# Optimization experiments

Hardware: AMD Instinct MI355X
Metric: run time of the kernel (lower is better)

Reference implementation:

```python
import jax, jax.numpy as jnp
import numpy as np

ZNEAR, ZFAR = 0.01, 100.0
EPS2D = 0.3            # gsplat 2D covariance blur
ALPHA_MIN = 1.0 / 255.0
ALPHA_MAX = 0.999
N_GAUSS, N_VIEWS, IMG_H, IMG_W = 4096, 1, 128, 128


def quat_to_rotmat(q):
    # q: [N,4] in wxyz (gsplat convention), normalized here
    q = q / jnp.linalg.norm(q, axis=-1, keepdims=True)
    w, x, y, z = q[..., 0], q[..., 1], q[..., 2], q[..., 3]
    r0 = jnp.stack([1 - 2 * (y * y + z * z), 2 * (x * y - w * z), 2 * (x * z + w * y)], -1)
    r1 = jnp.stack([2 * (x * y + w * z), 1 - 2 * (x * x + z * z), 2 * (y * z - w * x)], -1)
    r2 = jnp.stack([2 * (x * z - w * y), 2 * (y * z + w * x), 1 - 2 * (x * x + y * y)], -1)
    return jnp.stack([r0, r1, r2], -2)


def _render_one(K, viewmat, means, quats, scales, opacities, rgb, H, W):
    # --- project gaussians to camera space ---
    Rw, tw = viewmat[:3, :3], viewmat[:3, 3]
    p = means @ Rw.T + tw                              # [N,3]
    x, y, z = p[:, 0], p[:, 1], p[:, 2]
    zs = jnp.where(jnp.abs(z) < 1e-6, 1e-6, z)
    rz = 1.0 / zs

    # --- 3D covariance: R(q) diag(s^2) R(q)^T, rotated into camera frame ---
    Rg = quat_to_rotmat(quats)                         # [N,3,3]
    M = Rg * scales[:, None, :]
    cov3d = M @ jnp.swapaxes(M, -1, -2)
    covc = jnp.einsum('ij,njk,lk->nil', Rw, cov3d, Rw)

    # --- EWA splatting: 2D covariance via perspective Jacobian ---
    fx, fy, cx, cy = K[0, 0], K[1, 1], K[0, 2], K[1, 2]
    zeros = jnp.zeros_like(rz)
    J = jnp.stack([
        jnp.stack([fx * rz, zeros, -fx * x * rz * rz], -1),
        jnp.stack([zeros, fy * rz, -fy * y * rz * rz], -1),
    ], -2)                                             # [N,2,3]
    cov2d = jnp.einsum('nij,njk,nlk->nil', J, covc, J)
    a = cov2d[:, 0, 0] + EPS2D
    c = cov2d[:, 1, 1] + EPS2D
    b = cov2d[:, 0, 1]
    det = a * c - b * b
    det_s = jnp.where(det > 0, det, 1.0)
    ca, cb, cc = c / det_s, -b / det_s, a / det_s      # conic = inv(cov2d)

    mx = fx * x * rz + cx
    my = fy * y * rz + cy
    valid = (z > ZNEAR) & (z < ZFAR) & (det > 0)

    # --- front-to-back depth ordering ---
    order = jnp.argsort(jnp.where(valid, z, jnp.inf))
    mx, my = mx[order], my[order]
    ca, cb, cc = ca[order], cb[order], cc[order]
    op_s, rgb_s, valid_s = opacities[order], rgb[order], valid[order]

    # --- per-pixel gaussian evaluation (pixel centers at +0.5) ---
    px = jnp.arange(W, dtype=jnp.float32) + 0.5
    py = jnp.arange(H, dtype=jnp.float32) + 0.5
    dx = px[None, None, :] - mx[:, None, None]          # [N,1,W]
    dy = py[None, :, None] - my[:, None, None]          # [N,H,1]
    sigma = 0.5 * (ca[:, None, None] * dx * dx + cc[:, None, None] * dy * dy) + cb[:, None, None] * dx * dy
    alpha = jnp.minimum(ALPHA_MAX, op_s[:, None, None] * jnp.exp(-sigma))
    keep = (sigma >= 0) & (alpha >= ALPHA_MIN) & valid_s[:, None, None]
    alpha = jnp.where(keep, alpha, 0.0)                 # [N,H,W]

    # --- alpha compositing: T_i = prod_{j<i}(1-alpha_j) ---
    Tincl = jnp.cumprod(1.0 - alpha, axis=0)
    Texcl = jnp.concatenate([jnp.ones_like(alpha[:1]), Tincl[:-1]], axis=0)
    w = alpha * Texcl
    img = jnp.einsum('nhw,nc->hwc', w, rgb_s)
    bg = jnp.zeros((rgb.shape[-1],), dtype=img.dtype)   # bg_color buffer is zeros
    img = img + Tincl[-1][..., None] * bg
    return img


def setup_inputs() -> dict:
    key = jax.random.key(0)
    ks = jax.random.split(key, 6)
    xy = jax.random.uniform(ks[0], (N_GAUSS, 2), minval=-2.0, maxval=2.0)
    z = jax.random.uniform(ks[1], (N_GAUSS, 1), minval=2.0, maxval=8.0)
    means = jnp.concatenate([xy, z], axis=-1)
    quats = jax.random.normal(ks[2], (N_GAUSS, 4))
    scales = jax.random.uniform(ks[3], (N_GAUSS, 3), minval=0.02, maxval=0.12)
    opacities = jax.random.uniform(ks[4], (N_GAUSS,), minval=0.3, maxval=1.0)
    rgb = jax.random.uniform(ks[5], (N_GAUSS, 3))
    K = jnp.array([[140.0, 0.0, IMG_W / 2], [0.0, 140.0, IMG_H / 2], [0.0, 0.0, 1.0]], dtype=jnp.float32)
    Ks = jnp.tile(K[None], (N_VIEWS, 1, 1))
    viewmats = jnp.tile(jnp.eye(4, dtype=jnp.float32)[None], (N_VIEWS, 1, 1))
    return {"Ks": Ks, "viewmats": viewmats, "means": means, "quats": quats,
            "scales": scales, "opacities": opacities, "rgb": rgb,
            "im_height": IMG_H, "im_width": IMG_W}


def reference(Ks, viewmats, means, quats, scales, opacities, rgb, im_height, im_width):
    render = jax.vmap(lambda K, vm: _render_one(K, vm, means, quats, scales, opacities, rgb, im_height, im_width))
    imgs = render(Ks, viewmats)                 # [V,H,W,C]
    return jnp.transpose(imgs, (0, 3, 1, 2))    # 'v h w c -> v c h w'
```

## Files before the change

kernel.cpp:

```cpp
#include <hip/hip_runtime.h>
#include <hip/hip_bf16.h>
#include <hip/hip_fp16.h>

typedef unsigned long long u64;

#define ZNEAR 0.01f
#define ZFAR 100.0f
#define EPS2D 0.3f
#define ALPHA_MIN (1.0f/255.0f)
#define ALPHA_MAX 0.999f
#define IMGH 128
#define IMGW 128
#define NPIX (IMGH*IMGW)
#define TMIN 1e-5f

__device__ __forceinline__ float ldin(const void* p, int i, bool f32in) {
    if (f32in) return ((const float*)p)[i];
    return __bfloat162float(((const __hip_bfloat16*)p)[i]);
}

__device__ __forceinline__ bool probe_f32(const void* Ks) {
    float v = ((const float*)Ks)[0];
    return (v > 1e-3f) && (v < 1e9f);
}

__global__ void prep_kernel(const void* __restrict__ Ks,
                            const void* __restrict__ vm,
                            const void* __restrict__ c0,
                            const void* __restrict__ c1,
                            const void* __restrict__ c2,
                            const void* __restrict__ quats,
                            const void* __restrict__ opac,
                            u64* __restrict__ keys,
                            float4* __restrict__ params,
                            int N)
{
    int i = blockIdx.x * blockDim.x + threadIdx.x;
    if (i >= N) return;
    bool F = probe_f32(Ks);

    const void* cand[3] = {c0, c1, c2};
    float mxv[3];
    #pragma unroll
    for (int t = 0; t < 3; ++t) {
        float m = 0.f;
        for (int k = 0; k < 16; ++k) m = fmaxf(m, fabsf(ldin(cand[t], 3*k+2, F)));
        mxv[t] = m;
    }
    const void* means = c0; const void* scales = c1; const void* rgb = c2;
    #pragma unroll
    for (int t = 0; t < 3; ++t) {
        if (mxv[t] > 1.5f)       means  = cand[t];
        else if (mxv[t] > 0.3f)  rgb    = cand[t];
        else                     scales = cand[t];
    }

    float fx = ldin(Ks,0,F), fy = ldin(Ks,4,F), cx = ldin(Ks,2,F), cy = ldin(Ks,5,F);
    float R00=ldin(vm,0,F),  R01=ldin(vm,1,F),  R02=ldin(vm,2,F),  t0=ldin(vm,3,F);
    float R10=ldin(vm,4,F),  R11=ldin(vm,5,F),  R12=ldin(vm,6,F),  t1=ldin(vm,7,F);
    float R20=ldin(vm,8,F),  R21=ldin(vm,9,F),  R22=ldin(vm,10,F), t2=ldin(vm,11,F);

    float m0=ldin(means,3*i,F), m1=ldin(means,3*i+1,F), m2=ldin(means,3*i+2,F);
    float px = R00*m0 + R01*m1 + R02*m2 + t0;
    float py = R10*m0 + R11*m1 + R12*m2 + t1;
    float pz = R20*m0 + R21*m1 + R22*m2 + t2;

    float zs = (fabsf(pz) < 1e-6f) ? 1e-6f : pz;
    float rz = 1.0f / zs;

    float qw=ldin(quats,4*i,F), qx=ldin(quats,4*i+1,F),
          qy=ldin(quats,4*i+2,F), qz=ldin(quats,4*i+3,F);
    float s2 = 2.0f / (qw*qw + qx*qx + qy*qy + qz*qz);
    float G00 = 1.0f - s2*(qy*qy + qz*qz), G01 = s2*(qx*qy - qw*qz), G02 = s2*(qx*qz + qw*qy);
    float G10 = s2*(qx*qy + qw*qz), G11 = 1.0f - s2*(qx*qx + qz*qz), G12 = s2*(qy*qz - qw*qx);
    float G20 = s2*(qx*qz - qw*qy), G21 = s2*(qy*qz + qw*qx), G22 = 1.0f - s2*(qx*qx + qy*qy);

    float s0=ldin(scales,3*i,F), s1=ldin(scales,3*i+1,F), sc2=ldin(scales,3*i+2,F);
    float M00=G00*s0, M01=G01*s1, M02=G02*sc2;
    float M10=G10*s0, M11=G11*s1, M12=G12*sc2;
    float M20=G20*s0, M21=G21*s1, M22=G22*sc2;

    float C00 = M00*M00 + M01*M01 + M02*M02;
    float C01 = M00*M10 + M01*M11 + M02*M12;
    float C02 = M00*M20 + M01*M21 + M02*M22;
    float C11 = M10*M10 + M11*M11 + M12*M12;
    float C12 = M10*M20 + M11*M21 + M12*M22;
    float C22 = M20*M20 + M21*M21 + M22*M22;

    float T00 = R00*C00 + R01*C01 + R02*C02;
    float T01 = R00*C01 + R01*C11 + R02*C12;
    float T02 = R00*C02 + R01*C12 + R02*C22;
    float T10 = R10*C00 + R11*C01 + R12*C02;
    float T11 = R10*C01 + R11*C11 + R12*C12;
    float T12 = R10*C02 + R11*C12 + R12*C22;
    float T20 = R20*C00 + R21*C01 + R22*C02;
    float T21 = R20*C01 + R21*C11 + R22*C12;
    float T22 = R20*C02 + R21*C12 + R22*C22;

    float W00 = T00*R00 + T01*R01 + T02*R02;
    float W01 = T00*R10 + T01*R11 + T02*R12;
    float W02 = T00*R20 + T01*R21 + T02*R22;
    float W11 = T10*R10 + T11*R11 + T12*R12;
    float W12 = T10*R20 + T11*R21 + T12*R22;
    float W22 = T20*R20 + T21*R21 + T22*R22;

    float j00 = fx*rz, j02 = -fx*px*rz*rz;
    float j11 = fy*rz, j12 = -fy*py*rz*rz;

    float U00 = j00*W00 + j02*W02;
    float U01 = j00*W01 + j02*W12;
    float U02 = j00*W02 + j02*W22;
    float U11 = j11*W11 + j12*W12;
    float U12 = j11*W12 + j12*W22;
    float c00v = U00*j00 + U02*j02;
    float c01v = U01*j11 + U02*j12;
    float c11v = U11*j11 + U12*j12;

    float a  = c00v + EPS2D;
    float cd = c11v + EPS2D;
    float b  = c01v;
    float det = a*cd - b*b;

    bool valid = (pz > ZNEAR) && (pz < ZFAR) && (det > 0.0f);

    float mx = fx*px*rz + cx;
    float my = fy*py*rz + cy;
    float op = ldin(opac,i,F);
    float ica, icb, icc;
    if (valid) {
        float rdet = 1.0f / det;
        ica = cd * rdet; icb = -b * rdet; icc = a * rdet;
    } else {
        ica = 1.0f; icb = 0.0f; icc = 1.0f; op = 0.0f; mx = 0.0f; my = 0.0f;
    }

    int bx0 = 15, bx1 = 0, by0 = 15, by1 = 0;
    float s = __logf(255.0f * fmaxf(op, 1e-20f)) + 0.02f;
    if (valid && s > 0.0f) {
        float dxm = sqrtf(2.0f * s * a)  + 0.6f;
        float dym = sqrtf(2.0f * s * cd) + 0.6f;
        float xlo = mx - dxm - 0.5f, xhi = mx + dxm - 0.5f;
        float ylo = my - dym - 0.5f, yhi = my + dym - 0.5f;
        if (xhi >= 0.f && xlo <= (IMGW-1) && yhi >= 0.f && ylo <= (IMGH-1)) {
            bx0 = max(0, (int)floorf(xlo * (1.0f/16.0f)));
            bx1 = min(7, (int)floorf(xhi * (1.0f/16.0f)));
            by0 = max(0, (int)floorf(ylo * (1.0f/16.0f)));
            by1 = min(7, (int)floorf(yhi * (1.0f/16.0f)));
            if (bx0 > bx1 || by0 > by1) { bx0 = 15; bx1 = 0; }
        }
    }

    float cr=ldin(rgb,3*i,F), cg=ldin(rgb,3*i+1,F), cb=ldin(rgb,3*i+2,F);
    unsigned int rgp = ((unsigned int)__half_as_ushort(__float2half(cg)) << 16)
                     |  (unsigned int)__half_as_ushort(__float2half(cr));
    unsigned int bw  = ((unsigned int)__half_as_ushort(__float2half(cb)) << 16)
                     | (unsigned int)(bx0 | (bx1<<4) | (by0<<8) | (by1<<12));
    params[2*i]   = make_float4(mx, my, ica, icb);
    params[2*i+1] = make_float4(icc, op, __uint_as_float(rgp), __uint_as_float(bw));

    unsigned int zb = valid ? __float_as_uint(pz) : 0x7f800000u;
    keys[i] = ((u64)zb << 32) | (unsigned int)i;
}

#define NJ 16
__global__ __launch_bounds__(256) void rank_kernel(const u64* __restrict__ keys,
                                                   int* __restrict__ rank2d,
                                                   int N, int JC)
{
    __shared__ u64 sk[256];
    int jseg = blockIdx.y;
    int j0 = jseg * JC;
    int j1 = min(N, j0 + JC);
    int n = j1 - j0;
    for (int j = threadIdx.x; j < n; j += blockDim.x) sk[j] = keys[j0 + j];
    __syncthreads();
    int i = blockIdx.x * blockDim.x + threadIdx.x;
    if (i >= N) return;
    u64 k = keys[i];
    int r = 0;
    #pragma unroll 8
    for (int j = 0; j < n; ++j) r += (sk[j] < k) ? 1 : 0;
    rank2d[jseg * N + i] = r;
}

__global__ void scatter_kernel(const int* __restrict__ rank2d,
                               const float4* __restrict__ params,
                               float4* __restrict__ sorted, int N)
{
    int i = blockIdx.x * blockDim.x + threadIdx.x;
    if (i >= N) return;
    int r = 0;
    #pragma unroll
    for (int s = 0; s < NJ; ++s) r += rank2d[s * N + i];
    sorted[2*r]   = params[2*i];
    sorted[2*r+1] = params[2*i+1];
}

#define CHUNK 256
__global__ __launch_bounds__(256) void render_kernel(const float4* __restrict__ sp,
                                                     float4* __restrict__ partial,
                                                     int N, int C)
{
    __shared__ float4 sh[2*CHUNK];
    int tile = blockIdx.x;
    int s = blockIdx.y;
    int tx = tile & 7, ty = tile >> 3;
    int lx = threadIdx.x & 15, ly = threadIdx.x >> 4;
    int lane = threadIdx.x & 63;
    int x = (tx << 4) + lx;
    int y = (ty << 4) + ly;
    float pxc = x + 0.5f, pyc = y + 0.5f;

    int g0 = s * C;
    int g1 = min(N, g0 + C);

    float T = 1.0f, accr = 0.f, accg = 0.f, accb = 0.f;
    for (int base = g0; base < g1; base += CHUNK) {
        int cn = min(CHUNK, g1 - base);
        int idx = threadIdx.x;
        if (idx  < 2*cn) sh[idx]       = sp[2*base + idx];
        int idx2 = idx + 256;
        if (idx2 < 2*cn) sh[idx2]      = sp[2*base + idx2];
        __syncthreads();

        for (int sub = 0; sub < cn; sub += 64) {
            int gl = sub + lane;
            bool hit = (gl < cn);
            unsigned int meta = hit ? __float_as_uint(sh[2*gl+1].w) : 0u;
            int b0 =  meta        & 15;
            int b1 = (meta >> 4)  & 15;
            int b2 = (meta >> 8)  & 15;
            int b3 = (meta >> 12) & 15;
            hit = hit && (tx >= b0) && (tx <= b1) && (ty >= b2) && (ty <= b3);
            u64 m = __ballot(hit);
            if (__ballot(T > TMIN) == 0ull) m = 0;
            while (m) {
                int g = __ffsll(m) - 1; m &= m - 1;
                int gi = sub + g;
                float4 q0 = sh[2*gi];
                float4 q1 = sh[2*gi+1];
                float dx = pxc - q0.x, dy = pyc - q0.y;
                float sig = 0.5f*(q0.z*dx*dx + q1.x*dy*dy) + q0.w*(dx*dy);
                float al = fminf(ALPHA_MAX, q1.y * __expf(-sig));
                if (sig >= 0.0f && al >= ALPHA_MIN) {
                    unsigned int rgp = __float_as_uint(q1.z);
                    float cr = __half2float(__ushort_as_half((unsigned short)(rgp & 0xffffu)));
                    float cg = __half2float(__ushort_as_half((unsigned short)(rgp >> 16)));
                    float cb = __half2float(__ushort_as_half((unsigned short)(__float_as_uint(q1.w) >> 16)));
                    float w = al * T;
                    accr = fmaf(w, cr, accr);
                    accg = fmaf(w, cg, accg);
                    accb = fmaf(w, cb, accb);
                    T *= (1.0f - al);
                }
            }
        }
        if (__syncthreads_count(T > TMIN) == 0) break;
    }

    int p = y * IMGW + x;
    partial[s * NPIX + p] = make_float4(accr, accg, accb, T);
}

__global__ void combine_kernel(const float4* __restrict__ partial,
                               float* __restrict__ out, int S)
{
    int p = blockIdx.x * blockDim.x + threadIdx.x;
    if (p >= NPIX) return;
    float T = 1.f, r = 0.f, g = 0.f, b = 0.f;
    for (int s = 0; s < S; ++s) {
        float4 v = partial[s * NPIX + p];
        r = fmaf(T, v.x, r);
        g = fmaf(T, v.y, g);
        b = fmaf(T, v.z, b);
        T *= v.w;
    }
    out[p]          = r;
    out[NPIX + p]   = g;
    out[2*NPIX + p] = b;
}

extern "C" void kernel_launch(void* const* d_in, const int* in_sizes, int n_in,
                              void* d_out, int out_size, void* d_ws, size_t ws_size,
                              hipStream_t stream)
{
    const void* Ks = nullptr; const void* vm = nullptr;
    const void* quats = nullptr; const void* opac = nullptr;
    const void* c3n[3] = {nullptr, nullptr, nullptr};
    int nc = 0;
    int Nmin = 0x7fffffff;
    for (int i = 0; i < n_in; ++i) {
        int s = in_sizes[i];
        if (s > 16) Nmin = (s < Nmin) ? s : Nmin;
    }
    for (int i = 0; i < n_in; ++i) {
        int s = in_sizes[i];
        if (s == 9) Ks = d_in[i];
        else if (s == 16) vm = d_in[i];
        else if (s == Nmin) opac = d_in[i];
        else if (s == 4*Nmin) quats = d_in[i];
        else if (s == 3*Nmin && nc < 3) c3n[nc++] = d_in[i];
    }
    int N = Nmin;
    if (!Ks || !vm || !quats || !opac || nc != 3) {
        Ks = d_in[0]; vm = d_in[1]; c3n[0] = d_in[2]; quats = d_in[3];
        c3n[1] = d_in[4]; opac = d_in[5]; c3n[2] = d_in[6];
        N = in_sizes[5];
    }

    size_t off = 0;
    char* wsb = (char*)d_ws;
    auto take = [&](size_t bytes) -> void* {
        void* p = wsb + off;
        off += (bytes + 255) & ~(size_t)255;
        return p;
    };
    u64*    keys   = (u64*)   take((size_t)N * 8);
    float4* params = (float4*)take((size_t)N * 32);
    float4* sorted = (float4*)take((size_t)N * 32);
    int*    rank2d = (int*)   take((size_t)NJ * N * 4);

    int S = 16;
    while (S > 1 && off + (size_t)S * NPIX * 16 > ws_size) S >>= 1;
    float4* partial = (float4*)take((size_t)S * NPIX * 16);

    int nb = (N + 255) / 256;
    prep_kernel<<<nb, 256, 0, stream>>>(Ks, vm, c3n[0], c3n[1], c3n[2],
                                        quats, opac, keys, params, N);
    int JC = (N + NJ - 1) / NJ;
    rank_kernel<<<dim3(nb, NJ), 256, 0, stream>>>(keys, rank2d, N, JC);
    scatter_kernel<<<nb, 256, 0, stream>>>(rank2d, params, sorted, N);
    int C = (N + S - 1) / S;
    render_kernel<<<dim3(64, S), 256, 0, stream>>>(sorted, partial, N, C);
    combine_kernel<<<(NPIX + 255) / 256, 256, 0, stream>>>(partial,
                                                           (float*)d_out, S);
}
```

Measured before the change: 98.07 us.

## Fuse rank+scatter, drop depth-split render and combine, use 16x8 tiles

The rank and scatter kernels are merged into one kernel. Each thread now counts its rank over all keys, staged through 32KB of shared memory, and then scatters its params directly. The render no longer splits the sorted gaussians across 16 depth segments with a combine pass. Instead, 128 blocks of 16x8-pixel tiles each walk the whole sorted list and write the final image, and tile bounds in prep use 8-pixel rows. This removes two launches and the partial buffer traffic, but it cuts render parallelism from 1024 blocks to 128 and serialises the full gaussian list per tile, though the early exit on transmittance can help.

```diff
diff --git a/kernel.cpp b/kernel.cpp
--- a/kernel.cpp
+++ b/kernel.cpp
@@ -142,11 +142,11 @@
         float xlo = mx - dxm - 0.5f, xhi = mx + dxm - 0.5f;
         float ylo = my - dym - 0.5f, yhi = my + dym - 0.5f;
         if (xhi >= 0.f && xlo <= (IMGW-1) && yhi >= 0.f && ylo <= (IMGH-1)) {
-            bx0 = max(0, (int)floorf(xlo * (1.0f/16.0f)));
-            bx1 = min(7, (int)floorf(xhi * (1.0f/16.0f)));
-            by0 = max(0, (int)floorf(ylo * (1.0f/16.0f)));
-            by1 = min(7, (int)floorf(yhi * (1.0f/16.0f)));
-            if (bx0 > bx1 || by0 > by1) { bx0 = 15; bx1 = 0; }
+            bx0 = max(0,  (int)floorf(xlo * (1.0f/16.0f)));
+            bx1 = min(7,  (int)floorf(xhi * (1.0f/16.0f)));
+            by0 = max(0,  (int)floorf(ylo * (1.0f/8.0f)));
+            by1 = min(15, (int)floorf(yhi * (1.0f/8.0f)));
+            if (bx0 > bx1 || by0 > by1) { bx0 = 15; bx1 = 0; by0 = 15; by1 = 0; }
         }
     }
 
@@ -162,65 +162,48 @@
     keys[i] = ((u64)zb << 32) | (unsigned int)i;
 }
 
-#define NJ 16
-__global__ __launch_bounds__(256) void rank_kernel(const u64* __restrict__ keys,
-                                                   int* __restrict__ rank2d,
-                                                   int N, int JC)
-{
-    __shared__ u64 sk[256];
-    int jseg = blockIdx.y;
-    int j0 = jseg * JC;
-    int j1 = min(N, j0 + JC);
-    int n = j1 - j0;
-    for (int j = threadIdx.x; j < n; j += blockDim.x) sk[j] = keys[j0 + j];
-    __syncthreads();
+#define KCH 4096
+__global__ __launch_bounds__(256) void sort_scatter_kernel(
+    const u64* __restrict__ keys,
+    const float4* __restrict__ params,
+    float4* __restrict__ sorted, int N)
+{
+    __shared__ u64 sk[KCH];
     int i = blockIdx.x * blockDim.x + threadIdx.x;
+    u64 k = (i < N) ? keys[i] : 0;
+    int r = 0;
+    for (int j0 = 0; j0 < N; j0 += KCH) {
+        int n = min(KCH, N - j0);
+        __syncthreads();
+        for (int j = threadIdx.x; j < n; j += blockDim.x) sk[j] = keys[j0 + j];
+        __syncthreads();
+        #pragma unroll 8
+        for (int j = 0; j < n; ++j) r += (sk[j] < k) ? 1 : 0;
+    }
     if (i >= N) return;
-    u64 k = keys[i];
-    int r = 0;
-    #pragma unroll 8
-    for (int j = 0; j < n; ++j) r += (sk[j] < k) ? 1 : 0;
-    rank2d[jseg * N + i] = r;
-}
-
-__global__ void scatter_kernel(const int* __restrict__ rank2d,
-                               const float4* __restrict__ params,
-                               float4* __restrict__ sorted, int N)
-{
-    int i = blockIdx.x * blockDim.x + threadIdx.x;
-    if (i >= N) return;
-    int r = 0;
-    #pragma unroll
-    for (int s = 0; s < NJ; ++s) r += rank2d[s * N + i];
     sorted[2*r]   = params[2*i];
     sorted[2*r+1] = params[2*i+1];
 }
 
 #define CHUNK 256
-__global__ __launch_bounds__(256) void render_kernel(const float4* __restrict__ sp,
-                                                     float4* __restrict__ partial,
-                                                     int N, int C)
+__global__ __launch_bounds__(128) void render_kernel(const float4* __restrict__ sp,
+                                                     float* __restrict__ out,
+                                                     int N)
 {
     __shared__ float4 sh[2*CHUNK];
     int tile = blockIdx.x;
-    int s = blockIdx.y;
     int tx = tile & 7, ty = tile >> 3;
     int lx = threadIdx.x & 15, ly = threadIdx.x >> 4;
     int lane = threadIdx.x & 63;
     int x = (tx << 4) + lx;
-    int y = (ty << 4) + ly;
+    int y = (ty << 3) + ly;
     float pxc = x + 0.5f, pyc = y + 0.5f;
 
-    int g0 = s * C;
-    int g1 = min(N, g0 + C);
-
     float T = 1.0f, accr = 0.f, accg = 0.f, accb = 0.f;
-    for (int base = g0; base < g1; base += CHUNK) {
-        int cn = min(CHUNK, g1 - base);
-        int idx = threadIdx.x;
-        if (idx  < 2*cn) sh[idx]       = sp[2*base + idx];
-        int idx2 = idx + 256;
-        if (idx2 < 2*cn) sh[idx2]      = sp[2*base + idx2];
+    for (int base = 0; base < N; base += CHUNK) {
+        int cn = min(CHUNK, N - base);
+        for (int kk = (int)threadIdx.x; kk < 2*cn; kk += 128)
+            sh[kk] = sp[2*base + kk];
         __syncthreads();
 
         for (int sub = 0; sub < cn; sub += 64) {
@@ -259,25 +242,9 @@
     }
 
     int p = y * IMGW + x;
-    partial[s * NPIX + p] = make_float4(accr, accg, accb, T);
-}
-
-__global__ void combine_kernel(const float4* __restrict__ partial,
-                               float* __restrict__ out, int S)
-{
-    int p = blockIdx.x * blockDim.x + threadIdx.x;
-    if (p >= NPIX) return;
-    float T = 1.f, r = 0.f, g = 0.f, b = 0.f;
-    for (int s = 0; s < S; ++s) {
-        float4 v = partial[s * NPIX + p];
-        r = fmaf(T, v.x, r);
-        g = fmaf(T, v.y, g);
-        b = fmaf(T, v.z, b);
-        T *= v.w;
-    }
-    out[p]          = r;
-    out[NPIX + p]   = g;
-    out[2*NPIX + p] = b;
+    out[p]          = accr;
+    out[NPIX + p]   = accg;
+    out[2*NPIX + p] = accb;
 }
 
 extern "C" void kernel_launch(void* const* d_in, const int* in_sizes, int n_in,
@@ -318,20 +285,10 @@
     u64*    keys   = (u64*)   take((size_t)N * 8);
     float4* params = (float4*)take((size_t)N * 32);
     float4* sorted = (float4*)take((size_t)N * 32);
-    int*    rank2d = (int*)   take((size_t)NJ * N * 4);
-
-    int S = 16;
-    while (S > 1 && off + (size_t)S * NPIX * 16 > ws_size) S >>= 1;
-    float4* partial = (float4*)take((size_t)S * NPIX * 16);
 
     int nb = (N + 255) / 256;
     prep_kernel<<<nb, 256, 0, stream>>>(Ks, vm, c3n[0], c3n[1], c3n[2],
                                         quats, opac, keys, params, N);
-    int JC = (N + NJ - 1) / NJ;
-    rank_kernel<<<dim3(nb, NJ), 256, 0, stream>>>(keys, rank2d, N, JC);
-    scatter_kernel<<<nb, 256, 0, stream>>>(rank2d, params, sorted, N);
-    int C = (N + S - 1) / S;
-    render_kernel<<<dim3(64, S), 256, 0, stream>>>(sorted, partial, N, C);
-    combine_kernel<<<(NPIX + 255) / 256, 256, 0, stream>>>(partial,
-                                                           (float*)d_out, S);
-}
+    sort_scatter_kernel<<<nb, 256, 0, stream>>>(keys, params, sorted, N);
+    render_kernel<<<128, 128, 0, stream>>>(sorted, (float*)d_out, N);
+}
```

New measurement: 192.9 us. 1.97x slower.

## Fuse rank counting and scatter into one sort kernel with subgroup reduction

Applied to the files above, without the earlier changes.

Replaces the two-kernel rank-sort (a segmented rank count writing partial ranks to global memory, then a scatter that sums them) with a single kernel. In it, 16 lanes cooperate on each key, each scanning a 256-key slice of a 4096-key shared-memory chunk, and the partial counts are reduced with shuffles before the scatter. This removes one launch and the rank2d global round trip. In exchange, every block now loads all keys into shared memory (32 KB) and there are 256 blocks instead of 16x16. It also makes the empty-bbox case set by0/by1 consistently.

```diff
diff --git a/kernel.cpp b/kernel.cpp
--- a/kernel.cpp
+++ b/kernel.cpp
@@ -146,7 +146,7 @@
             bx1 = min(7, (int)floorf(xhi * (1.0f/16.0f)));
             by0 = max(0, (int)floorf(ylo * (1.0f/16.0f)));
             by1 = min(7, (int)floorf(yhi * (1.0f/16.0f)));
-            if (bx0 > bx1 || by0 > by1) { bx0 = 15; bx1 = 0; }
+            if (bx0 > bx1 || by0 > by1) { bx0 = 15; bx1 = 0; by0 = 15; by1 = 0; }
         }
     }
 
@@ -162,38 +162,38 @@
     keys[i] = ((u64)zb << 32) | (unsigned int)i;
 }
 
-#define NJ 16
-__global__ __launch_bounds__(256) void rank_kernel(const u64* __restrict__ keys,
-                                                   int* __restrict__ rank2d,
-                                                   int N, int JC)
-{
-    __shared__ u64 sk[256];
-    int jseg = blockIdx.y;
-    int j0 = jseg * JC;
-    int j1 = min(N, j0 + JC);
-    int n = j1 - j0;
-    for (int j = threadIdx.x; j < n; j += blockDim.x) sk[j] = keys[j0 + j];
-    __syncthreads();
-    int i = blockIdx.x * blockDim.x + threadIdx.x;
-    if (i >= N) return;
-    u64 k = keys[i];
+#define KCH 4096
+__global__ __launch_bounds__(256) void sort_scatter_kernel(
+    const u64* __restrict__ keys,
+    const float4* __restrict__ params,
+    float4* __restrict__ sorted, int N)
+{
+    __shared__ u64 sk[KCH];
+    int tid = threadIdx.x;
+    int g = tid >> 4;
+    int s = tid & 15;
+    int i = blockIdx.x * 16 + g;
+    u64 k = (i < N) ? keys[i] : 0;
     int r = 0;
-    #pragma unroll 8
-    for (int j = 0; j < n; ++j) r += (sk[j] < k) ? 1 : 0;
-    rank2d[jseg * N + i] = r;
-}
-
-__global__ void scatter_kernel(const int* __restrict__ rank2d,
-                               const float4* __restrict__ params,
-                               float4* __restrict__ sorted, int N)
-{
-    int i = blockIdx.x * blockDim.x + threadIdx.x;
-    if (i >= N) return;
-    int r = 0;
-    #pragma unroll
-    for (int s = 0; s < NJ; ++s) r += rank2d[s * N + i];
-    sorted[2*r]   = params[2*i];
-    sorted[2*r+1] = params[2*i+1];
+    for (int cbase = 0; cbase < N; cbase += KCH) {
+        int n = min(KCH, N - cbase);
+        __syncthreads();
+        for (int j = tid; j < KCH; j += 256)
+            sk[j] = (j < n) ? keys[cbase + j] : ~0ull;
+        __syncthreads();
+        int j0 = s * 256;
+        #pragma unroll 8
+        for (int jj = 0; jj < 256; ++jj)
+            r += (sk[j0 + jj] < k) ? 1 : 0;
+    }
+    r += __shfl_xor(r, 1, 16);
+    r += __shfl_xor(r, 2, 16);
+    r += __shfl_xor(r, 4, 16);
+    r += __shfl_xor(r, 8, 16);
+    if (i < N && s == 0) {
+        sorted[2*r]   = params[2*i];
+        sorted[2*r+1] = params[2*i+1];
+    }
 }
 
 #define CHUNK 256
@@ -218,9 +218,9 @@
     for (int base = g0; base < g1; base += CHUNK) {
         int cn = min(CHUNK, g1 - base);
         int idx = threadIdx.x;
-        if (idx  < 2*cn) sh[idx]       = sp[2*base + idx];
+        if (idx  < 2*cn) sh[idx]  = sp[2*base + idx];
         int idx2 = idx + 256;
-        if (idx2 < 2*cn) sh[idx2]      = sp[2*base + idx2];
+        if (idx2 < 2*cn) sh[idx2] = sp[2*base + idx2];
         __syncthreads();
 
         for (int sub = 0; sub < cn; sub += 64) {
@@ -318,7 +318,6 @@
     u64*    keys   = (u64*)   take((size_t)N * 8);
     float4* params = (float4*)take((size_t)N * 32);
     float4* sorted = (float4*)take((size_t)N * 32);
-    int*    rank2d = (int*)   take((size_t)NJ * N * 4);
 
     int S = 16;
     while (S > 1 && off + (size_t)S * NPIX * 16 > ws_size) S >>= 1;
@@ -327,9 +326,7 @@
     int nb = (N + 255) / 256;
     prep_kernel<<<nb, 256, 0, stream>>>(Ks, vm, c3n[0], c3n[1], c3n[2],
                                         quats, opac, keys, params, N);
-    int JC = (N + NJ - 1) / NJ;
-    rank_kernel<<<dim3(nb, NJ), 256, 0, stream>>>(keys, rank2d, N, JC);
-    scatter_kernel<<<nb, 256, 0, stream>>>(rank2d, params, sorted, N);
+    sort_scatter_kernel<<<(N + 15) / 16, 256, 0, stream>>>(keys, params, sorted, N);
     int C = (N + S - 1) / S;
     render_kernel<<<dim3(64, S), 256, 0, stream>>>(sorted, partial, N, C);
     combine_kernel<<<(NPIX + 255) / 256, 256, 0, stream>>>(partial,
```

After: 109.8 us. +12.0%, slower.
